# Kernel tuning notes

Hardware: AMD Instinct MI355X
Metric: run time of the kernel (lower is better)

The kernel has to match this reference:

```python
import jax, jax.numpy as jnp
import numpy as np

B, S, D_IN = 2, 2048, 1024
H, DA, DH = 16, 64, 64          # num_heads, attention_dim, head_dim (linear_hidden_dim)
EMBED = 1024
KSIZE = 1


def causal_conv1d(x_bsc, w):
    """x_bsc: (B,S,Cin); w: (Cout,Cin,K). Left-pad K-1 -> causal. Returns (B,Cout,S)."""
    k = w.shape[-1]
    x_bcs = jnp.transpose(x_bsc, (0, 2, 1))
    x_bcs = jnp.pad(x_bcs, ((0, 0), (0, 0), (k - 1, 0)))
    return jax.lax.conv_general_dilated(
        x_bcs, w, window_strides=(1,), padding='VALID',
        dimension_numbers=('NCH', 'OIH', 'NCH'))


def setup_inputs() -> dict:
    key = jax.random.key(0)
    ks = jax.random.split(key, 7)
    x = jax.random.normal(ks[0], (B, S, D_IN), dtype=jnp.float32)
    # causal mask: 1 where attended, 0 where masked (masked_fill where ==0)
    attn_mask = jnp.tril(jnp.ones((S, S), dtype=jnp.int32))[None, None]  # (1,1,S,S)
    wq = 0.02 * jax.random.normal(ks[1], (H * DA, D_IN, KSIZE), dtype=jnp.float32)
    wk = 0.02 * jax.random.normal(ks[2], (H * DA, D_IN, KSIZE), dtype=jnp.float32)
    wv = 0.02 * jax.random.normal(ks[3], (H * DH, D_IN, KSIZE), dtype=jnp.float32)
    w_out = 0.02 * jax.random.normal(ks[4], (EMBED, H * DH), dtype=jnp.float32)
    b_out = 0.02 * jax.random.normal(ks[5], (EMBED,), dtype=jnp.float32)
    return {"x": x, "attn_mask": attn_mask, "wq": wq, "wk": wk, "wv": wv,
            "w_out": w_out, "b_out": b_out}


def reference(x, attn_mask, wq, wk, wv, w_out, b_out):
    b, s, _ = x.shape
    scale = DH ** (-0.5)  # NOTE: torch code scales by head_dim, not attention_dim
    q = causal_conv1d(x, wq)  # (B, H*DA, S)
    k = causal_conv1d(x, wk)  # (B, H*DA, S)
    v = causal_conv1d(x, wv)  # (B, H*DH, S)
    q = q.reshape(b, H, DA, s).transpose(0, 1, 3, 2)  # (B,H,S,DA)
    k = k.reshape(b, H, DA, s).transpose(0, 1, 3, 2)
    v = v.reshape(b, H, DH, s).transpose(0, 1, 3, 2)  # (B,H,S,DH)
    scores = scale * jnp.einsum('bhnd,bhmd->bhnm', q, k)
    scores = jnp.where(attn_mask == 0, -jnp.inf, scores)
    probs = jax.nn.softmax(scores, axis=-1)
    context = jnp.einsum('bhnm,bhmd->bhnd', probs, v)  # (B,H,S,DH)
    context = context.transpose(0, 2, 1, 3).reshape(b, s, H * DH)
    return context @ w_out.T + b_out
```

## Files before the change

kernel.cpp:

```cpp
#include <hip/hip_runtime.h>
#include <math.h>


typedef __bf16 bf16;
typedef __bf16 bf16x8 __attribute__((ext_vector_type(8)));
typedef __bf16 bf16x4 __attribute__((ext_vector_type(4)));
typedef float  f32x4  __attribute__((ext_vector_type(4)));

#define MFMA16(a, b, c) __builtin_amdgcn_mfma_f32_16x16x32_bf16((a), (b), (c), 0, 0, 0)

__device__ __forceinline__ void gll16(const void* g, void* l) {
    __builtin_amdgcn_global_load_lds(
        (__attribute__((address_space(1))) unsigned int*)g,
        (__attribute__((address_space(3))) unsigned int*)l, 16, 0, 0);
}

__global__ __launch_bounds__(256) void cvt_all_kernel(
    const float* __restrict__ x,  const float* __restrict__ wq,
    const float* __restrict__ wk, const float* __restrict__ wv,
    const float* __restrict__ wo,
    bf16* __restrict__ xb,  bf16* __restrict__ wqb, bf16* __restrict__ wkb,
    bf16* __restrict__ wvb, bf16* __restrict__ wob)
{
    const int blk = blockIdx.x;
    const float* src; bf16* dst; int off; float scale = 1.f;
    if (blk < 4096)      { src = x;  dst = xb;  off = blk * 1024; }
    else if (blk < 5120) { src = wq; dst = wqb; off = (blk - 4096) * 1024;
                           scale = 0.18033688011112042f; }
    else if (blk < 6144) { src = wk; dst = wkb; off = (blk - 5120) * 1024; }
    else if (blk < 7168) { src = wv; dst = wvb; off = (blk - 6144) * 1024; }
    else                 { src = wo; dst = wob; off = (blk - 7168) * 1024; }
    const int i = off + threadIdx.x * 4;
    f32x4 v = *(const f32x4*)(src + i);
    bf16x4 o;
    o[0] = (bf16)(v[0] * scale); o[1] = (bf16)(v[1] * scale);
    o[2] = (bf16)(v[2] * scale); o[3] = (bf16)(v[3] * scale);
    *(bf16x4*)(dst + i) = o;
}

__global__ __launch_bounds__(256, 3) void qkv_mfma_kernel(
    const bf16* __restrict__ xb, const bf16* __restrict__ wqb,
    const bf16* __restrict__ wkb, const bf16* __restrict__ wvb,
    bf16* __restrict__ Qb, bf16* __restrict__ Kb, bf16* __restrict__ Vtb)
{
    __shared__ bf16 As[2][128 * 32];
    __shared__ bf16 Bs[2][128 * 32];
    const int mt = blockIdx.x;
    const int nt = blockIdx.y;
    const int which = nt >> 3;
    const bf16* Wm = (which == 0) ? wqb : (which == 1) ? wkb : wvb;

    const int t = threadIdx.x;
    const int w = t >> 6, lane = t & 63, quad = lane >> 4, l16 = lane & 15;
    const int wm = (w >> 1) * 64, wn = (w & 1) * 64;
    const int srow = lane >> 2;
    const int scol = (lane & 3) * 8;

    const bf16* Ab = xb + ((size_t)(mt * 128) + srow) * 1024 + scol;
    const bf16* Bb = Wm + ((size_t)((nt & 7) * 128) + srow) * 1024 + scol;

    f32x4 acc[4][4];
    #pragma unroll
    for (int i = 0; i < 4; i++)
        #pragma unroll
        for (int j = 0; j < 4; j++)
            #pragma unroll
            for (int r = 0; r < 4; r++) acc[i][j][r] = 0.f;

    gll16(Ab + (size_t)(w * 16) * 1024,       As[0] + w * 512);
    gll16(Ab + (size_t)((w + 4) * 16) * 1024, As[0] + (w + 4) * 512);
    gll16(Bb + (size_t)(w * 16) * 1024,       Bs[0] + w * 512);
    gll16(Bb + (size_t)((w + 4) * 16) * 1024, Bs[0] + (w + 4) * 512);

    for (int it = 0; it < 32; it++) {
        const int cur = it & 1, nxt = cur ^ 1;
        __syncthreads();
        if (it < 31) {
            const int kn = it * 32 + 32;
            gll16(Ab + (size_t)(w * 16) * 1024 + kn,       As[nxt] + w * 512);
            gll16(Ab + (size_t)((w + 4) * 16) * 1024 + kn, As[nxt] + (w + 4) * 512);
            gll16(Bb + (size_t)(w * 16) * 1024 + kn,       Bs[nxt] + w * 512);
            gll16(Bb + (size_t)((w + 4) * 16) * 1024 + kn, Bs[nxt] + (w + 4) * 512);
        }
        bf16x8 af[4], bfr[4];
        #pragma unroll
        for (int i = 0; i < 4; i++)
            af[i] = *(const bf16x8*)&As[cur][(wm + i * 16 + l16) * 32 + quad * 8];
        #pragma unroll
        for (int j = 0; j < 4; j++)
            bfr[j] = *(const bf16x8*)&Bs[cur][(wn + j * 16 + l16) * 32 + quad * 8];
        #pragma unroll
        for (int i = 0; i < 4; i++)
            #pragma unroll
            for (int j = 0; j < 4; j++)
                acc[i][j] = MFMA16(af[i], bfr[j], acc[i][j]);
    }

    const int nbase = (nt & 7) * 128 + wn;
    if (which == 2) {
        #pragma unroll
        for (int i = 0; i < 4; i++) {
            const int m0 = mt * 128 + wm + i * 16 + quad * 4;
            const int bb = m0 >> 11, s0 = m0 & 2047;
            #pragma unroll
            for (int j = 0; j < 4; j++) {
                const int n = nbase + j * 16 + l16;
                const int h = n >> 6, d = n & 63;
                bf16x4 pk;
                #pragma unroll
                for (int r = 0; r < 4; r++) pk[r] = (bf16)acc[i][j][r];
                *(bf16x4*)&Vtb[(((size_t)(bb * 16 + h)) * 64 + d) * 2048 + s0] = pk;
            }
        }
    } else {
        bf16* Out = (which == 0) ? Qb : Kb;
        #pragma unroll
        for (int i = 0; i < 4; i++) {
            #pragma unroll
            for (int r = 0; r < 4; r++) {
                const int m = mt * 128 + wm + i * 16 + quad * 4 + r;
                const int bb = m >> 11, s = m & 2047;
                #pragma unroll
                for (int j = 0; j < 4; j++) {
                    const int n = nbase + j * 16 + l16;
                    const int h = n >> 6, d = n & 63;
                    Out[(((size_t)(bb * 16 + h)) * 2048 + s) * 64 + d] =
                        (bf16)acc[i][j][r];
                }
            }
        }
    }
}

__global__ __launch_bounds__(256, 2) void attn_mfma_kernel(
    const bf16* __restrict__ Qb, const bf16* __restrict__ Kb,
    const bf16* __restrict__ Vtb, bf16* __restrict__ ctxb)
{
    __shared__ bf16 Ks[2][64 * 64];
    __shared__ bf16 Vts[2][64 * 64];
    __shared__ bf16 Pl[4][16 * 72];

    const int id = blockIdx.x;
    const int bh = id & 31;
    const int g = id >> 5;
    const int u = ((g & 7) << 1) | ((bh >> 4) & 1);
    const int tsel = ((bh >> 3) ^ (g >> 3)) & 1;
    const int qt = tsel ? (15 - u) : u;
    const int h = bh & 15, b = bh >> 4;
    const int t = threadIdx.x;
    const int w = t >> 6, lane = t & 63, quad = lane >> 4, l16 = lane & 15;
    const int sr = lane >> 3, sc = lane & 7;

    const size_t hb = (size_t)(b * 16 + h);
    const bf16* Qh = Qb + hb * (2048 * 64);
    const bf16* Kh = Kb + hb * (2048 * 64);
    const bf16* Vh = Vtb + hb * (64 * 2048);

    bf16x8 qf[2][2];
    #pragma unroll
    for (int rt = 0; rt < 2; rt++) {
        const bf16* Qrow = Qh + (size_t)(qt * 128 + w * 32 + rt * 16 + l16) * 64;
        qf[rt][0] = *(const bf16x8*)(Qrow + quad * 8);
        qf[rt][1] = *(const bf16x8*)(Qrow + 32 + quad * 8);
    }

    {
        const int r0 = w * 8 + sr, r1 = (w + 4) * 8 + sr;
        gll16(Kh + (size_t)r0 * 64 + (sc ^ sr) * 8, Ks[0] + w * 512);
        gll16(Kh + (size_t)r1 * 64 + (sc ^ sr) * 8, Ks[0] + (w + 4) * 512);
        gll16(Vh + (size_t)r0 * 2048 + (sc ^ sr) * 8, Vts[0] + w * 512);
        gll16(Vh + (size_t)r1 * 2048 + (sc ^ sr) * 8, Vts[0] + (w + 4) * 512);
    }

    bf16x8 ones;
    #pragma unroll
    for (int i = 0; i < 8; i++) ones[i] = (bf16)1.0f;

    f32x4 o_acc[2][4], l_acc[2];
    #pragma unroll
    for (int rt = 0; rt < 2; rt++) {
        #pragma unroll
        for (int r = 0; r < 4; r++) l_acc[rt][r] = 0.f;
        #pragma unroll
        for (int dt = 0; dt < 4; dt++)
            #pragma unroll
            for (int r = 0; r < 4; r++) o_acc[rt][dt][r] = 0.f;
    }

    const int ktmax = 2 * qt + 1;
    for (int kt = 0; kt <= ktmax; kt++) {
        const int cur = kt & 1, nxt = cur ^ 1;
        __syncthreads();
        if (kt < ktmax) {
            const int kn = kt + 1;
            const int r0 = w * 8 + sr, r1 = (w + 4) * 8 + sr;
            gll16(Kh + (size_t)(kn * 64 + r0) * 64 + (sc ^ sr) * 8, Ks[nxt] + w * 512);
            gll16(Kh + (size_t)(kn * 64 + r1) * 64 + (sc ^ sr) * 8, Ks[nxt] + (w + 4) * 512);
            gll16(Vh + (size_t)r0 * 2048 + kn * 64 + (sc ^ sr) * 8, Vts[nxt] + w * 512);
            gll16(Vh + (size_t)r1 * 2048 + kn * 64 + (sc ^ sr) * 8, Vts[nxt] + (w + 4) * 512);
        }

        f32x4 sacc[2][4];
        #pragma unroll
        for (int rt = 0; rt < 2; rt++)
            #pragma unroll
            for (int tt = 0; tt < 4; tt++)
                #pragma unroll
                for (int r = 0; r < 4; r++) sacc[rt][tt][r] = 0.f;
        #pragma unroll
        for (int tt = 0; tt < 4; tt++) {
            const int krow = tt * 16 + l16;
            bf16x8 kf0 = *(const bf16x8*)&Ks[cur][krow * 64 + ((quad)     ^ (krow & 7)) * 8];
            bf16x8 kf1 = *(const bf16x8*)&Ks[cur][krow * 64 + ((quad + 4) ^ (krow & 7)) * 8];
            #pragma unroll
            for (int rt = 0; rt < 2; rt++) {
                sacc[rt][tt] = MFMA16(kf0, qf[rt][0], sacc[rt][tt]);
                sacc[rt][tt] = MFMA16(kf1, qf[rt][1], sacc[rt][tt]);
            }
        }

        bf16x8 bv[4][2];
        #pragma unroll
        for (int dt = 0; dt < 4; dt++) {
            const int drow = dt * 16 + l16;
            bv[dt][0] = *(const bf16x8*)&Vts[cur][drow * 64 + ((quad)     ^ (drow & 7)) * 8];
            bv[dt][1] = *(const bf16x8*)&Vts[cur][drow * 64 + ((quad + 4) ^ (drow & 7)) * 8];
        }

        const bool diag = (kt >= 2 * qt);
        #pragma unroll
        for (int rt = 0; rt < 2; rt++) {
            const int qrow = qt * 128 + w * 32 + rt * 16 + l16;
            #pragma unroll
            for (int tt = 0; tt < 4; tt++) {
                bf16x4 pk;
                #pragma unroll
                for (int r = 0; r < 4; r++) {
                    float p = __builtin_amdgcn_exp2f(sacc[rt][tt][r]);
                    if (diag && (kt * 64 + tt * 16 + quad * 4 + r) > qrow) p = 0.f;
                    pk[r] = (bf16)p;
                }
                *(bf16x4*)&Pl[w][l16 * 72 + tt * 16 + quad * 4] = pk;
            }
            bf16x8 ap0 = *(const bf16x8*)&Pl[w][l16 * 72 + quad * 8];
            bf16x8 ap1 = *(const bf16x8*)&Pl[w][l16 * 72 + 32 + quad * 8];
            l_acc[rt] = MFMA16(ap0, ones, l_acc[rt]);
            l_acc[rt] = MFMA16(ap1, ones, l_acc[rt]);
            #pragma unroll
            for (int dt = 0; dt < 4; dt++) {
                o_acc[rt][dt] = MFMA16(ap0, bv[dt][0], o_acc[rt][dt]);
                o_acc[rt][dt] = MFMA16(ap1, bv[dt][1], o_acc[rt][dt]);
            }
        }
    }

    #pragma unroll
    for (int rt = 0; rt < 2; rt++)
        #pragma unroll
        for (int r = 0; r < 4; r++) {
            const float inv = 1.f / l_acc[rt][r];
            const int s = qt * 128 + w * 32 + rt * 16 + quad * 4 + r;
            #pragma unroll
            for (int dt = 0; dt < 4; dt++)
                ctxb[((size_t)(b * 2048 + s)) * 1024 + h * 64 + dt * 16 + l16] =
                    (bf16)(o_acc[rt][dt][r] * inv);
        }
}

__global__ __launch_bounds__(256, 2) void oproj_mfma_kernel(
    const bf16* __restrict__ ctxb, const bf16* __restrict__ wob,
    const float* __restrict__ b_out, float* __restrict__ out)
{
    __shared__ bf16 As[2][64 * 32];
    __shared__ bf16 Bs[2][128 * 32];
    const int mt = blockIdx.x;
    const int nt = blockIdx.y;
    const int t = threadIdx.x;
    const int w = t >> 6, lane = t & 63, quad = lane >> 4, l16 = lane & 15;
    const int srow = lane >> 2;
    const int scol = (lane & 3) * 8;

    const bf16* Ab = ctxb + (size_t)(mt * 64 + srow) * 1024 + scol;
    const bf16* Bb = wob + (size_t)(nt * 128 + srow) * 1024 + scol;

    f32x4 acc[8];
    #pragma unroll
    for (int j = 0; j < 8; j++)
        #pragma unroll
        for (int r = 0; r < 4; r++) acc[j][r] = 0.f;

    gll16(Ab + (size_t)(w * 16) * 1024,       As[0] + w * 512);
    gll16(Bb + (size_t)(w * 16) * 1024,       Bs[0] + w * 512);
    gll16(Bb + (size_t)((w + 4) * 16) * 1024, Bs[0] + (w + 4) * 512);

    for (int it = 0; it < 32; it++) {
        const int cur = it & 1, nxt = cur ^ 1;
        __syncthreads();
        if (it < 31) {
            const int kn = it * 32 + 32;
            gll16(Ab + (size_t)(w * 16) * 1024 + kn,       As[nxt] + w * 512);
            gll16(Bb + (size_t)(w * 16) * 1024 + kn,       Bs[nxt] + w * 512);
            gll16(Bb + (size_t)((w + 4) * 16) * 1024 + kn, Bs[nxt] + (w + 4) * 512);
        }
        bf16x8 af = *(const bf16x8*)&As[cur][(w * 16 + l16) * 32 + quad * 8];
        #pragma unroll
        for (int j = 0; j < 8; j++) {
            bf16x8 bfr = *(const bf16x8*)&Bs[cur][(j * 16 + l16) * 32 + quad * 8];
            acc[j] = MFMA16(af, bfr, acc[j]);
        }
    }

    #pragma unroll
    for (int j = 0; j < 8; j++)
        #pragma unroll
        for (int r = 0; r < 4; r++) {
            const int m = mt * 64 + w * 16 + quad * 4 + r;
            const int n = nt * 128 + j * 16 + l16;
            out[(size_t)m * 1024 + n] = acc[j][r] + b_out[n];
        }
}

extern "C" void kernel_launch(void* const* d_in, const int* in_sizes, int n_in,
                              void* d_out, int out_size, void* d_ws, size_t ws_size,
                              hipStream_t stream)
{
    const float* x     = (const float*)d_in[0];
    const float* wq    = (const float*)d_in[2];
    const float* wk    = (const float*)d_in[3];
    const float* wv    = (const float*)d_in[4];
    const float* w_out = (const float*)d_in[5];
    const float* b_out = (const float*)d_in[6];
    float* out = (float*)d_out;

    char* ws = (char*)d_ws;
    bf16* xb   = (bf16*)(ws);
    bf16* wqb  = (bf16*)(ws + (8u  << 20));
    bf16* wkb  = (bf16*)(ws + (10u << 20));
    bf16* wvb  = (bf16*)(ws + (12u << 20));
    bf16* wob  = (bf16*)(ws + (14u << 20));
    bf16* Qb   = (bf16*)(ws + (16u << 20));
    bf16* Kb   = (bf16*)(ws + (24u << 20));
    bf16* Vtb  = (bf16*)(ws + (32u << 20));
    bf16* ctxb = (bf16*)(ws + (40u << 20));

    cvt_all_kernel<<<8192, 256, 0, stream>>>(x, wq, wk, wv, w_out,
                                             xb, wqb, wkb, wvb, wob);
    qkv_mfma_kernel<<<dim3(32, 24), 256, 0, stream>>>(xb, wqb, wkb, wvb, Qb, Kb, Vtb);
    attn_mfma_kernel<<<512, 256, 0, stream>>>(Qb, Kb, Vtb, ctxb);
    oproj_mfma_kernel<<<dim3(64, 8), 256, 0, stream>>>(ctxb, wob, b_out, out);
}
```

Baseline: 196.8 us.

## Stream K/V from global into registers and trim causal tiles per wave

The attention kernel no longer stages K and V tiles in shared memory with async global-to-LDS loads and block-wide barriers. Each wave now loads K fragments straight into registers, double-buffered across key tiles, and reads V fragments directly from global memory. Each wave also computes its own key-tile count from its 32 query rows, so it skips fully masked tiles, and the P scratch buffer gets a swizzled per-row-tile layout. The aim is to remove barrier stalls and wasted causal work, at the cost of redundant global/L2 reads, since all four waves fetch the same K/V, and higher register pressure.

```diff
diff --git a/kernel.cpp b/kernel.cpp
--- a/kernel.cpp
+++ b/kernel.cpp
@@ -136,42 +136,32 @@
     const bf16* __restrict__ Qb, const bf16* __restrict__ Kb,
     const bf16* __restrict__ Vtb, bf16* __restrict__ ctxb)
 {
-    __shared__ bf16 Ks[2][64 * 64];
-    __shared__ bf16 Vts[2][64 * 64];
-    __shared__ bf16 Pl[4][16 * 72];
+    __shared__ bf16 Pl[8][16 * 64];
 
     const int id = blockIdx.x;
     const int bh = id & 31;
     const int g = id >> 5;
-    const int u = ((g & 7) << 1) | ((bh >> 4) & 1);
-    const int tsel = ((bh >> 3) ^ (g >> 3)) & 1;
-    const int qt = tsel ? (15 - u) : u;
+    const int qt = (g < 8) ? g : (23 - g);
     const int h = bh & 15, b = bh >> 4;
     const int t = threadIdx.x;
     const int w = t >> 6, lane = t & 63, quad = lane >> 4, l16 = lane & 15;
-    const int sr = lane >> 3, sc = lane & 7;
+    const int e8 = l16 & 7;
 
     const size_t hb = (size_t)(b * 16 + h);
     const bf16* Qh = Qb + hb * (2048 * 64);
     const bf16* Kh = Kb + hb * (2048 * 64);
     const bf16* Vh = Vtb + hb * (64 * 2048);
 
+    const int qbase = qt * 128 + w * 32;
+
     bf16x8 qf[2][2];
     #pragma unroll
     for (int rt = 0; rt < 2; rt++) {
-        const bf16* Qrow = Qh + (size_t)(qt * 128 + w * 32 + rt * 16 + l16) * 64;
+        const bf16* Qrow = Qh + (size_t)(qbase + rt * 16 + l16) * 64;
         qf[rt][0] = *(const bf16x8*)(Qrow + quad * 8);
         qf[rt][1] = *(const bf16x8*)(Qrow + 32 + quad * 8);
     }
 
-    {
-        const int r0 = w * 8 + sr, r1 = (w + 4) * 8 + sr;
-        gll16(Kh + (size_t)r0 * 64 + (sc ^ sr) * 8, Ks[0] + w * 512);
-        gll16(Kh + (size_t)r1 * 64 + (sc ^ sr) * 8, Ks[0] + (w + 4) * 512);
-        gll16(Vh + (size_t)r0 * 2048 + (sc ^ sr) * 8, Vts[0] + w * 512);
-        gll16(Vh + (size_t)r1 * 2048 + (sc ^ sr) * 8, Vts[0] + (w + 4) * 512);
-    }
-
     bf16x8 ones;
     #pragma unroll
     for (int i = 0; i < 8; i++) ones[i] = (bf16)1.0f;
@@ -187,79 +177,90 @@
             for (int r = 0; r < 4; r++) o_acc[rt][dt][r] = 0.f;
     }
 
-    const int ktmax = 2 * qt + 1;
-    for (int kt = 0; kt <= ktmax; kt++) {
-        const int cur = kt & 1, nxt = cur ^ 1;
-        __syncthreads();
-        if (kt < ktmax) {
-            const int kn = kt + 1;
-            const int r0 = w * 8 + sr, r1 = (w + 4) * 8 + sr;
-            gll16(Kh + (size_t)(kn * 64 + r0) * 64 + (sc ^ sr) * 8, Ks[nxt] + w * 512);
-            gll16(Kh + (size_t)(kn * 64 + r1) * 64 + (sc ^ sr) * 8, Ks[nxt] + (w + 4) * 512);
-            gll16(Vh + (size_t)r0 * 2048 + kn * 64 + (sc ^ sr) * 8, Vts[nxt] + w * 512);
-            gll16(Vh + (size_t)r1 * 2048 + kn * 64 + (sc ^ sr) * 8, Vts[nxt] + (w + 4) * 512);
-        }
-
-        f32x4 sacc[2][4];
-        #pragma unroll
-        for (int rt = 0; rt < 2; rt++)
-            #pragma unroll
-            for (int tt = 0; tt < 4; tt++)
-                #pragma unroll
-                for (int r = 0; r < 4; r++) sacc[rt][tt][r] = 0.f;
-        #pragma unroll
-        for (int tt = 0; tt < 4; tt++) {
-            const int krow = tt * 16 + l16;
-            bf16x8 kf0 = *(const bf16x8*)&Ks[cur][krow * 64 + ((quad)     ^ (krow & 7)) * 8];
-            bf16x8 kf1 = *(const bf16x8*)&Ks[cur][krow * 64 + ((quad + 4) ^ (krow & 7)) * 8];
-            #pragma unroll
-            for (int rt = 0; rt < 2; rt++) {
-                sacc[rt][tt] = MFMA16(kf0, qf[rt][0], sacc[rt][tt]);
-                sacc[rt][tt] = MFMA16(kf1, qf[rt][1], sacc[rt][tt]);
-            }
-        }
-
-        bf16x8 bv[4][2];
-        #pragma unroll
-        for (int dt = 0; dt < 4; dt++) {
-            const int drow = dt * 16 + l16;
-            bv[dt][0] = *(const bf16x8*)&Vts[cur][drow * 64 + ((quad)     ^ (drow & 7)) * 8];
-            bv[dt][1] = *(const bf16x8*)&Vts[cur][drow * 64 + ((quad + 4) ^ (drow & 7)) * 8];
-        }
-
-        const bool diag = (kt >= 2 * qt);
-        #pragma unroll
-        for (int rt = 0; rt < 2; rt++) {
-            const int qrow = qt * 128 + w * 32 + rt * 16 + l16;
-            #pragma unroll
-            for (int tt = 0; tt < 4; tt++) {
-                bf16x4 pk;
-                #pragma unroll
-                for (int r = 0; r < 4; r++) {
-                    float p = __builtin_amdgcn_exp2f(sacc[rt][tt][r]);
-                    if (diag && (kt * 64 + tt * 16 + quad * 4 + r) > qrow) p = 0.f;
-                    pk[r] = (bf16)p;
-                }
-                *(bf16x4*)&Pl[w][l16 * 72 + tt * 16 + quad * 4] = pk;
-            }
-            bf16x8 ap0 = *(const bf16x8*)&Pl[w][l16 * 72 + quad * 8];
-            bf16x8 ap1 = *(const bf16x8*)&Pl[w][l16 * 72 + 32 + quad * 8];
-            l_acc[rt] = MFMA16(ap0, ones, l_acc[rt]);
-            l_acc[rt] = MFMA16(ap1, ones, l_acc[rt]);
-            #pragma unroll
-            for (int dt = 0; dt < 4; dt++) {
-                o_acc[rt][dt] = MFMA16(ap0, bv[dt][0], o_acc[rt][dt]);
-                o_acc[rt][dt] = MFMA16(ap1, bv[dt][1], o_acc[rt][dt]);
-            }
-        }
-    }
+    const int nkt = (qbase + 95) >> 6;
+
+    bf16x8 kfA[8], kfB[8];
+
+    #define LOADK(ktv, dst)                                                   \
+        {                                                                     \
+            _Pragma("unroll")                                                 \
+            for (int tt = 0; tt < 4; tt++) {                                  \
+                const bf16* Kr =                                              \
+                    Kh + (size_t)((ktv) * 64 + tt * 16 + l16) * 64 + quad * 8;\
+                (dst)[tt * 2 + 0] = *(const bf16x8*)(Kr);                     \
+                (dst)[tt * 2 + 1] = *(const bf16x8*)(Kr + 32);                \
+            }                                                                 \
+        }
+
+    #define BODY(ktv, kf)                                                     \
+        {                                                                     \
+            bf16x8 bv[4][2];                                                  \
+            _Pragma("unroll")                                                 \
+            for (int dt = 0; dt < 4; dt++) {                                  \
+                const bf16* Vr =                                              \
+                    Vh + (size_t)(dt * 16 + l16) * 2048 + (ktv) * 64 + quad * 8;\
+                bv[dt][0] = *(const bf16x8*)(Vr);                             \
+                bv[dt][1] = *(const bf16x8*)(Vr + 32);                        \
+            }                                                                 \
+            _Pragma("unroll")                                                 \
+            for (int rt = 0; rt < 2; rt++) {                                  \
+                f32x4 sacc[4];                                                \
+                _Pragma("unroll")                                             \
+                for (int tt = 0; tt < 4; tt++) {                              \
+                    _Pragma("unroll")                                         \
+                    for (int r = 0; r < 4; r++) sacc[tt][r] = 0.f;            \
+                    sacc[tt] = MFMA16((kf)[tt * 2 + 0], qf[rt][0], sacc[tt]); \
+                    sacc[tt] = MFMA16((kf)[tt * 2 + 1], qf[rt][1], sacc[tt]); \
+                }                                                             \
+                bf16* Prt = &Pl[w * 2 + rt][0];                               \
+                const int R = qbase + rt * 16;                                \
+                const bool msk = ((ktv) * 64 + 63) > R;                       \
+                const int qrow = R + l16;                                     \
+                _Pragma("unroll")                                             \
+                for (int tt = 0; tt < 4; tt++) {                              \
+                    bf16x4 pk;                                                \
+                    _Pragma("unroll")                                         \
+                    for (int r = 0; r < 4; r++) {                             \
+                        float p = __builtin_amdgcn_exp2f(sacc[tt][r]);        \
+                        if (msk && ((ktv) * 64 + tt * 16 + quad * 4 + r) > qrow) \
+                            p = 0.f;                                          \
+                        pk[r] = (bf16)p;                                      \
+                    }                                                         \
+                    *(bf16x4*)&Prt[l16 * 64 +                                 \
+                        (((tt * 2 + (quad >> 1)) ^ e8) * 8 + (quad & 1) * 4)] = pk; \
+                }                                                             \
+                bf16x8 ap0 = *(const bf16x8*)&Prt[l16 * 64 + ((quad ^ e8) * 8)];      \
+                bf16x8 ap1 = *(const bf16x8*)&Prt[l16 * 64 + (((quad + 4) ^ e8) * 8)];\
+                l_acc[rt] = MFMA16(ap0, ones, l_acc[rt]);                     \
+                l_acc[rt] = MFMA16(ap1, ones, l_acc[rt]);                     \
+                _Pragma("unroll")                                             \
+                for (int dt = 0; dt < 4; dt++) {                              \
+                    o_acc[rt][dt] = MFMA16(ap0, bv[dt][0], o_acc[rt][dt]);    \
+                    o_acc[rt][dt] = MFMA16(ap1, bv[dt][1], o_acc[rt][dt]);    \
+                }                                                             \
+            }                                                                 \
+        }
+
+    LOADK(0, kfA);
+    int kt = 0;
+    while (kt < nkt) {
+        if (kt + 1 < nkt) LOADK(kt + 1, kfB);
+        BODY(kt, kfA);
+        kt++;
+        if (kt >= nkt) break;
+        if (kt + 1 < nkt) LOADK(kt + 1, kfA);
+        BODY(kt, kfB);
+        kt++;
+    }
+    #undef LOADK
+    #undef BODY
 
     #pragma unroll
     for (int rt = 0; rt < 2; rt++)
         #pragma unroll
         for (int r = 0; r < 4; r++) {
             const float inv = 1.f / l_acc[rt][r];
-            const int s = qt * 128 + w * 32 + rt * 16 + quad * 4 + r;
+            const int s = qbase + rt * 16 + quad * 4 + r;
             #pragma unroll
             for (int dt = 0; dt < 4; dt++)
                 ctxb[((size_t)(b * 2048 + s)) * 1024 + h * 64 + dt * 16 + l16] =
```

Result: slower. 221.9 us (+12.8%).
